# Optimization experiments

Hardware: AMD Instinct MI355X
Metric: run time of the kernel (lower is better)

Reference implementation:

```python
import jax, jax.numpy as jnp
import numpy as np

T, B, I, H, NC = 1024, 256, 128, 64, 10


def _lstm_cell(x_t, h, c, W_ih, W_hh, b):
    # PyTorch gate order: i, f, g, o. gates: [B, 4H]
    gates = x_t @ W_ih.T + h @ W_hh.T + b
    i, f, g, o = jnp.split(gates, 4, axis=-1)
    i = jax.nn.sigmoid(i)
    f = jax.nn.sigmoid(f)
    g = jnp.tanh(g)
    o = jax.nn.sigmoid(o)
    c = f * c + i * g
    h = o * jnp.tanh(c)
    return h, c


def setup_inputs() -> dict:
    key = jax.random.key(0)
    ks = jax.random.split(key, 12)
    s = 1.0 / np.sqrt(H)  # PyTorch LSTM init scale
    d = {
        "x": jax.random.normal(ks[0], (T, B, I), dtype=jnp.float32),
        # forward direction LSTM params
        "W_ih_f": jax.random.uniform(ks[1], (4 * H, I), minval=-s, maxval=s, dtype=jnp.float32),
        "W_hh_f": jax.random.uniform(ks[2], (4 * H, H), minval=-s, maxval=s, dtype=jnp.float32),
        "b_f": jax.random.uniform(ks[3], (4 * H,), minval=-s, maxval=s, dtype=jnp.float32),
        # reverse direction LSTM params
        "W_ih_r": jax.random.uniform(ks[4], (4 * H, I), minval=-s, maxval=s, dtype=jnp.float32),
        "W_hh_r": jax.random.uniform(ks[5], (4 * H, H), minval=-s, maxval=s, dtype=jnp.float32),
        "b_r": jax.random.uniform(ks[6], (4 * H,), minval=-s, maxval=s, dtype=jnp.float32),
        # MLP head: 2H -> 64 -> 32 -> NC
        "fc1_w": jax.random.normal(ks[7], (64, 2 * H), dtype=jnp.float32) * 0.05,
        "fc1_b": jnp.zeros((64,), dtype=jnp.float32),
        "fc2_w": jax.random.normal(ks[8], (32, 64), dtype=jnp.float32) * 0.05,
        "fc2_b": jnp.zeros((32,), dtype=jnp.float32),
        "fc3_w": jax.random.normal(ks[9], (NC, 32), dtype=jnp.float32) * 0.05,
        "fc3_b": jnp.zeros((NC,), dtype=jnp.float32),
    }
    return d


def _forward(x, W_ih_f, W_hh_f, b_f, W_ih_r, W_hh_r, b_r,
             fc1_w, fc1_b, fc2_w, fc2_b, fc3_w, fc3_b):
    Bsz = x.shape[1]
    h0 = jnp.zeros((Bsz, H), dtype=x.dtype)
    c0 = jnp.zeros((Bsz, H), dtype=x.dtype)

    # Forward direction: only the final hidden state is needed (output[-1] fwd half).
    def fwd_step(carry, x_t):
        h, c = carry
        h, c = _lstm_cell(x_t, h, c, W_ih_f, W_hh_f, b_f)
        return (h, c), None

    (h_fwd_last, _), _ = jax.lax.scan(fwd_step, (h0, c0), x)

    # Reverse direction: output[-1] reverse half is the hidden after processing
    # x[-1] first (reverse scan starts from the last timestep with zero state).
    h_bwd_last, _ = _lstm_cell(x[-1], h0, c0, W_ih_r, W_hh_r, b_r)

    h_cat = jnp.concatenate([h_fwd_last, h_bwd_last], axis=-1)  # [B, 2H]

    h1 = jax.nn.relu(h_cat @ fc1_w.T + fc1_b)
    h2 = jax.nn.relu(h1 @ fc2_w.T + fc2_b)
    out = h2 @ fc3_w.T + fc3_b  # [B, NC]
    return out


def reference(x, W_ih_f, W_hh_f, b_f, W_ih_r, W_hh_r, b_r,
              fc1_w, fc1_b, fc2_w, fc2_b, fc3_w, fc3_b):
    return _forward(x, W_ih_f, W_hh_f, b_f, W_ih_r, W_hh_r, b_r,
                    fc1_w, fc1_b, fc2_w, fc2_b, fc3_w, fc3_b)
```

## Files before the change

### kernel.cpp

```cpp
#include <hip/hip_runtime.h>
#include <math.h>

#define T_LEN 1024
#define B_SZ  256
#define I_SZ  128
#define H_SZ  64
#define G_SZ  256
#define SUB   32

typedef float f32x8 __attribute__((ext_vector_type(8)));

__device__ __forceinline__ float fast_tanh(float x) {
    float e = __expf(-2.0f * fabsf(x));
    float r = (1.0f - e) * __builtin_amdgcn_rcpf(1.0f + e);
    return copysignf(r, x);
}

#define LD8PIN(V, P)                                                        \
    {   float4 t0_ = *reinterpret_cast<const float4*>(P);                   \
        float4 t1_ = *reinterpret_cast<const float4*>((P) + 4);             \
        V = (f32x8){t0_.x, t0_.y, t0_.z, t0_.w, t1_.x, t1_.y, t1_.z, t1_.w};\
        asm volatile("" : "+v"(V)); }

#define HD(V, M)                                                            \
    {   const float4 ha_ = hp[2*(M)], hb_ = hp[2*(M) + 1];                  \
        a0 = fmaf(ha_.x, V[0], a0); a1 = fmaf(ha_.y, V[1], a1);             \
        a2 = fmaf(ha_.z, V[2], a2); a3 = fmaf(ha_.w, V[3], a3);             \
        a0 = fmaf(hb_.x, V[4], a0); a1 = fmaf(hb_.y, V[5], a1);             \
        a2 = fmaf(hb_.z, V[6], a2); a3 = fmaf(hb_.w, V[7], a3); }

__device__ __forceinline__ int swz(int c) { return c + 4 * (c >> 5); }

__global__ __launch_bounds__(256, 2) void xg_gemm(
    const float* __restrict__ xch,
    const float* __restrict__ W_ih,
    const float* __restrict__ bias,
    float* __restrict__ XG)
{
    const int tid = threadIdx.x;
    const int tx  = tid & 15;
    const int ty  = tid >> 4;
    const int mt  = blockIdx.x;
    const int nt  = blockIdx.y;

    __shared__ __align__(16) float as[32][140];
    __shared__ __align__(16) float bs[32][140];

    const int n0 = nt * 128 + tx * 8;
    float4 bia = *reinterpret_cast<const float4*>(&bias[n0]);
    float4 bib = *reinterpret_cast<const float4*>(&bias[n0 + 4]);

    float acc[8][8];
#pragma unroll
    for (int r = 0; r < 8; ++r)
#pragma unroll
        for (int cc = 0; cc < 8; ++cc) acc[r][cc] = 0.0f;

    const int srow = tid >> 3;
    const int skk  = (tid & 7) * 4;

    for (int ks = 0; ks < 4; ++ks) {
        const int k0 = ks * 32;
        __syncthreads();
#pragma unroll
        for (int i = 0; i < 4; ++i) {
            const int mr = srow + 32 * i;
            float4 xa = *reinterpret_cast<const float4*>(
                &xch[(size_t)(mt * 128 + mr) * I_SZ + k0 + skk]);
            as[skk + 0][swz(mr)] = xa.x; as[skk + 1][swz(mr)] = xa.y;
            as[skk + 2][swz(mr)] = xa.z; as[skk + 3][swz(mr)] = xa.w;
            float4 wa = *reinterpret_cast<const float4*>(
                &W_ih[(size_t)(nt * 128 + mr) * I_SZ + k0 + skk]);
            bs[skk + 0][swz(mr)] = wa.x; bs[skk + 1][swz(mr)] = wa.y;
            bs[skk + 2][swz(mr)] = wa.z; bs[skk + 3][swz(mr)] = wa.w;
        }
        __syncthreads();

#pragma unroll 8
        for (int kk = 0; kk < 32; ++kk) {
            const float4 a0 = *reinterpret_cast<const float4*>(&as[kk][swz(ty * 8)]);
            const float4 a1 = *reinterpret_cast<const float4*>(&as[kk][swz(ty * 8) + 4]);
            const float4 b0 = *reinterpret_cast<const float4*>(&bs[kk][swz(tx * 8)]);
            const float4 b1 = *reinterpret_cast<const float4*>(&bs[kk][swz(tx * 8) + 4]);
            const float av[8] = {a0.x, a0.y, a0.z, a0.w, a1.x, a1.y, a1.z, a1.w};
            const float bv[8] = {b0.x, b0.y, b0.z, b0.w, b1.x, b1.y, b1.z, b1.w};
#pragma unroll
            for (int r = 0; r < 8; ++r)
#pragma unroll
                for (int cc = 0; cc < 8; ++cc)
                    acc[r][cc] = fmaf(av[r], bv[cc], acc[r][cc]);
        }
    }

#pragma unroll
    for (int r = 0; r < 8; ++r) {
        const size_t m = (size_t)(mt * 128 + ty * 8 + r);
        float4 o0 = {acc[r][0] + bia.x, acc[r][1] + bia.y,
                     acc[r][2] + bia.z, acc[r][3] + bia.w};
        float4 o1 = {acc[r][4] + bib.x, acc[r][5] + bib.y,
                     acc[r][6] + bib.z, acc[r][7] + bib.w};
        *reinterpret_cast<float4*>(&XG[m * G_SZ + n0])     = o0;
        *reinterpret_cast<float4*>(&XG[m * G_SZ + n0 + 4]) = o1;
    }
}

__global__ __launch_bounds__(512, 1) void lstm_rec(
    const float* __restrict__ XG,
    const float* __restrict__ W_hh,
    float* __restrict__ h_state,
    float* __restrict__ c_state,
    int TC, int first)
{
    const int b    = blockIdx.x;
    const int t    = threadIdx.x;
    const int row  = t >> 1;
    const int half = t & 1;
    const int g    = row >> 6;
    const int w    = t >> 6;
    const int l    = t & 63;

    __shared__ __align__(16) float xgl[2][SUB][G_SZ];
    __shared__ __align__(16) float hsb[8][H_SZ];
    __shared__ float gs[2][G_SZ];

    const float* ur = W_hh + row * H_SZ + half * 32;
    f32x8 w0, w1, w2, w3;
    LD8PIN(w0, ur) LD8PIN(w1, ur + 8) LD8PIN(w2, ur + 16) LD8PIN(w3, ur + 24)

    float c = first ? 0.0f : c_state[b * H_SZ + l];
    hsb[w][l] = first ? 0.0f : h_state[b * H_SZ + l];

    {
        float* xf = &xgl[0][0][0];
#pragma unroll
        for (int i = 0; i < 4; ++i) {
            const int F = t + 512 * i;
            const int r = F >> 6, cw = F & 63;
            *reinterpret_cast<float4*>(xf + 4 * F) =
                *reinterpret_cast<const float4*>(
                    XG + ((size_t)r * B_SZ + b) * G_SZ + 4 * cw);
        }
    }
    __syncthreads();

    const bool isg = (g == 2);
    const int nsub = TC / SUB;
    int db = 0;
    float h = 0.0f;

    for (int sub = 0; sub < nsub; ++sub) {
        const int cur = sub & 1;
        if (sub + 1 < nsub) {
            float* xf = &xgl[cur ^ 1][0][0];
#pragma unroll
            for (int i = 0; i < 4; ++i) {
                const int F = t + 512 * i;
                const int r = (F >> 6) + (sub + 1) * SUB, cw = F & 63;
                *reinterpret_cast<float4*>(xf + 4 * F) =
                    *reinterpret_cast<const float4*>(
                        XG + ((size_t)r * B_SZ + b) * G_SZ + 4 * cw);
            }
        }

#pragma unroll 4
        for (int ts = 0; ts < SUB; ++ts) {
            const float xg = xgl[cur][ts][row];
            const float4* hp =
                reinterpret_cast<const float4*>(&hsb[w][half * 32]);
            float a0 = 0.0f, a1 = 0.0f, a2 = 0.0f, a3 = 0.0f;
            HD(w0, 0) HD(w1, 1) HD(w2, 2) HD(w3, 3)
            float acc = (a0 + a1) + (a2 + a3);
            acc += __shfl_xor(acc, 1, 64);
            acc += xg;

            const float arg = isg ? (-2.0f * acc) : (-acc);
            const float e = __expf(arg);
            const float r = __builtin_amdgcn_rcpf(1.0f + e);
            const float a = isg ? (1.0f - e) * r : r;

            if (half == 0) gs[db][row] = a;
            __syncthreads();

            const float ig = gs[db][l];
            const float fg = gs[db][H_SZ + l];
            const float gg = gs[db][2 * H_SZ + l];
            const float og = gs[db][3 * H_SZ + l];
            c = fmaf(fg, c, ig * gg);
            h = og * fast_tanh(c);
            hsb[w][l] = h;
            db ^= 1;
        }
    }

    if (t < H_SZ) {
        h_state[b * H_SZ + t] = h;
        c_state[b * H_SZ + t] = c;
    }
}

__global__ __launch_bounds__(256, 1) void lstm_tail(
    const float* __restrict__ x_last,
    const float* __restrict__ W_ih_r,
    const float* __restrict__ b_r,
    const float* __restrict__ h_fwd,
    const float* __restrict__ fc1_w,
    const float* __restrict__ fc1_b,
    const float* __restrict__ fc2_w,
    const float* __restrict__ fc2_b,
    const float* __restrict__ fc3_w,
    const float* __restrict__ fc3_b,
    float* __restrict__ out)
{
    const int b = blockIdx.x;
    const int j = threadIdx.x;

    __shared__ float xs[I_SZ];
    __shared__ float gs[G_SZ];
    __shared__ float hc[2 * H_SZ];
    __shared__ float h1[64];
    __shared__ float h2[32];

    if (j < I_SZ) xs[j] = x_last[(size_t)b * I_SZ + j];
    if (j < H_SZ) hc[j] = h_fwd[b * H_SZ + j];
    __syncthreads();

    float a0 = b_r[j], a1 = 0.0f, a2 = 0.0f, a3 = 0.0f;
    const float* wrow = W_ih_r + j * I_SZ;
#pragma unroll
    for (int kk = 0; kk < I_SZ; kk += 4) {
        float4 wv = *reinterpret_cast<const float4*>(wrow + kk);
        a0 = fmaf(xs[kk + 0], wv.x, a0);
        a1 = fmaf(xs[kk + 1], wv.y, a1);
        a2 = fmaf(xs[kk + 2], wv.z, a2);
        a3 = fmaf(xs[kk + 3], wv.w, a3);
    }
    const float acc = (a0 + a1) + (a2 + a3);
    const int gate = j >> 6;
    gs[j] = (gate == 2) ? tanhf(acc) : 1.0f / (1.0f + expf(-acc));
    __syncthreads();

    if (j < H_SZ) {
        const float cc = gs[j] * gs[2 * H_SZ + j];
        hc[H_SZ + j] = gs[3 * H_SZ + j] * tanhf(cc);
    }
    __syncthreads();

    if (j < 64) {
        float s0 = fc1_b[j], s1 = 0.0f, s2 = 0.0f, s3 = 0.0f;
        const float* w = fc1_w + j * 128;
#pragma unroll
    for (int kk = 0; kk < 128; kk += 4) {
            float4 wv = *reinterpret_cast<const float4*>(w + kk);
            s0 = fmaf(hc[kk + 0], wv.x, s0);
            s1 = fmaf(hc[kk + 1], wv.y, s1);
            s2 = fmaf(hc[kk + 2], wv.z, s2);
            s3 = fmaf(hc[kk + 3], wv.w, s3);
        }
        h1[j] = fmaxf((s0 + s1) + (s2 + s3), 0.0f);
    }
    __syncthreads();

    if (j < 32) {
        float s0 = fc2_b[j], s1 = 0.0f, s2 = 0.0f, s3 = 0.0f;
        const float* w = fc2_w + j * 64;
#pragma unroll
        for (int kk = 0; kk < 64; kk += 4) {
            float4 wv = *reinterpret_cast<const float4*>(w + kk);
            s0 = fmaf(h1[kk + 0], wv.x, s0);
            s1 = fmaf(h1[kk + 1], wv.y, s1);
            s2 = fmaf(h1[kk + 2], wv.z, s2);
            s3 = fmaf(h1[kk + 3], wv.w, s3);
        }
        h2[j] = fmaxf((s0 + s1) + (s2 + s3), 0.0f);
    }
    __syncthreads();

    if (j < 10) {
        float s = fc3_b[j];
#pragma unroll
        for (int kk = 0; kk < 32; ++kk) s = fmaf(h2[kk], fc3_w[j * 32 + kk], s);
        out[b * 10 + j] = s;
    }
}

extern "C" void kernel_launch(void* const* d_in, const int* in_sizes, int n_in,
                              void* d_out, int out_size, void* d_ws, size_t ws_size,
                              hipStream_t stream) {
    const float* x      = (const float*)d_in[0];
    const float* W_ih_f = (const float*)d_in[1];
    const float* W_hh_f = (const float*)d_in[2];
    const float* b_f    = (const float*)d_in[3];
    const float* W_ih_r = (const float*)d_in[4];
    const float* b_r    = (const float*)d_in[6];
    const float* fc1_w  = (const float*)d_in[7];
    const float* fc1_b  = (const float*)d_in[8];
    const float* fc2_w  = (const float*)d_in[9];
    const float* fc2_b  = (const float*)d_in[10];
    const float* fc3_w  = (const float*)d_in[11];
    const float* fc3_b  = (const float*)d_in[12];
    float* out = (float*)d_out;

    int TC = 1024;
    while (TC > 64 &&
           (size_t)TC * B_SZ * G_SZ * 4 + 2 * B_SZ * H_SZ * 4 > ws_size)
        TC >>= 1;

    float* XG      = (float*)d_ws;
    float* h_state = (float*)((char*)d_ws + (size_t)TC * B_SZ * G_SZ * 4);
    float* c_state = h_state + B_SZ * H_SZ;

    const int NCH = T_LEN / TC;
    for (int ch = 0; ch < NCH; ++ch) {
        const float* xch = x + (size_t)ch * TC * B_SZ * I_SZ;
        hipLaunchKernelGGL(xg_gemm, dim3(TC * B_SZ / 128, 2), dim3(256), 0,
                           stream, xch, W_ih_f, b_f, XG);
        hipLaunchKernelGGL(lstm_rec, dim3(B_SZ), dim3(512), 0, stream,
                           XG, W_hh_f, h_state, c_state, TC, ch == 0 ? 1 : 0);
    }

    const float* x_last = x + (size_t)(T_LEN - 1) * B_SZ * I_SZ;
    hipLaunchKernelGGL(lstm_tail, dim3(B_SZ), dim3(256), 0, stream,
                       x_last, W_ih_r, b_r, h_state,
                       fc1_w, fc1_b, fc2_w, fc2_b, fc3_w, fc3_b, out);
}
```

Baseline: 685.8 us.

## Broadcast hidden state via readlane and use one thread per gate row

The recurrent kernel drops from 512 to 256 threads per block, so each thread now holds a full 64-wide W_hh row in registers instead of half a row. The cross-lane shuffle that combined the two halves is removed. The hidden state is no longer written to and read back from a per-wave LDS buffer; each wave broadcasts h from its own lanes with readlane into scalar registers. This removes LDS traffic and a shuffle from the serial per-timestep critical path, at the cost of 64 serialized readlanes and longer per-thread FMA chains, plus doubled weight register pressure.

```diff
diff --git a/kernel.cpp b/kernel.cpp
--- a/kernel.cpp
+++ b/kernel.cpp
@@ -22,12 +22,23 @@
         V = (f32x8){t0_.x, t0_.y, t0_.z, t0_.w, t1_.x, t1_.y, t1_.z, t1_.w};\
         asm volatile("" : "+v"(V)); }
 
-#define HD(V, M)                                                            \
-    {   const float4 ha_ = hp[2*(M)], hb_ = hp[2*(M) + 1];                  \
-        a0 = fmaf(ha_.x, V[0], a0); a1 = fmaf(ha_.y, V[1], a1);             \
-        a2 = fmaf(ha_.z, V[2], a2); a3 = fmaf(ha_.w, V[3], a3);             \
-        a0 = fmaf(hb_.x, V[4], a0); a1 = fmaf(hb_.y, V[5], a1);             \
-        a2 = fmaf(hb_.z, V[6], a2); a3 = fmaf(hb_.w, V[7], a3); }
+#define RL8(V, K)                                                           \
+    {   unsigned r0_ = __builtin_amdgcn_readlane(hu, (K) + 0);              \
+        unsigned r1_ = __builtin_amdgcn_readlane(hu, (K) + 1);              \
+        unsigned r2_ = __builtin_amdgcn_readlane(hu, (K) + 2);              \
+        unsigned r3_ = __builtin_amdgcn_readlane(hu, (K) + 3);              \
+        a0 = fmaf(__uint_as_float(r0_), V[0], a0);                          \
+        a1 = fmaf(__uint_as_float(r1_), V[1], a1);                          \
+        a2 = fmaf(__uint_as_float(r2_), V[2], a2);                          \
+        a3 = fmaf(__uint_as_float(r3_), V[3], a3);                          \
+        unsigned r4_ = __builtin_amdgcn_readlane(hu, (K) + 4);              \
+        unsigned r5_ = __builtin_amdgcn_readlane(hu, (K) + 5);              \
+        unsigned r6_ = __builtin_amdgcn_readlane(hu, (K) + 6);              \
+        unsigned r7_ = __builtin_amdgcn_readlane(hu, (K) + 7);              \
+        a0 = fmaf(__uint_as_float(r4_), V[4], a0);                          \
+        a1 = fmaf(__uint_as_float(r5_), V[5], a1);                          \
+        a2 = fmaf(__uint_as_float(r6_), V[6], a2);                          \
+        a3 = fmaf(__uint_as_float(r7_), V[7], a3); }
 
 __device__ __forceinline__ int swz(int c) { return c + 4 * (c >> 5); }
 
@@ -104,37 +115,35 @@
     }
 }
 
-__global__ __launch_bounds__(512, 1) void lstm_rec(
+__global__ __launch_bounds__(256, 1) void lstm_rec(
     const float* __restrict__ XG,
     const float* __restrict__ W_hh,
     float* __restrict__ h_state,
     float* __restrict__ c_state,
     int TC, int first)
 {
-    const int b    = blockIdx.x;
-    const int t    = threadIdx.x;
-    const int row  = t >> 1;
-    const int half = t & 1;
-    const int g    = row >> 6;
-    const int w    = t >> 6;
-    const int l    = t & 63;
+    const int b = blockIdx.x;
+    const int t = threadIdx.x;
+    const int l = t & 63;
+    const int g = t >> 6;
+    const int row = t;
 
     __shared__ __align__(16) float xgl[2][SUB][G_SZ];
-    __shared__ __align__(16) float hsb[8][H_SZ];
     __shared__ float gs[2][G_SZ];
 
-    const float* ur = W_hh + row * H_SZ + half * 32;
-    f32x8 w0, w1, w2, w3;
-    LD8PIN(w0, ur) LD8PIN(w1, ur + 8) LD8PIN(w2, ur + 16) LD8PIN(w3, ur + 24)
-
+    const float* ur = W_hh + row * H_SZ;
+    f32x8 w0, w1, w2, w3, w4, w5, w6, w7;
+    LD8PIN(w0, ur)      LD8PIN(w1, ur +  8) LD8PIN(w2, ur + 16) LD8PIN(w3, ur + 24)
+    LD8PIN(w4, ur + 32) LD8PIN(w5, ur + 40) LD8PIN(w6, ur + 48) LD8PIN(w7, ur + 56)
+
+    float h = first ? 0.0f : h_state[b * H_SZ + l];
     float c = first ? 0.0f : c_state[b * H_SZ + l];
-    hsb[w][l] = first ? 0.0f : h_state[b * H_SZ + l];
 
     {
         float* xf = &xgl[0][0][0];
 #pragma unroll
-        for (int i = 0; i < 4; ++i) {
-            const int F = t + 512 * i;
+        for (int i = 0; i < 8; ++i) {
+            const int F = t + 256 * i;
             const int r = F >> 6, cw = F & 63;
             *reinterpret_cast<float4*>(xf + 4 * F) =
                 *reinterpret_cast<const float4*>(
@@ -146,15 +155,14 @@
     const bool isg = (g == 2);
     const int nsub = TC / SUB;
     int db = 0;
-    float h = 0.0f;
 
     for (int sub = 0; sub < nsub; ++sub) {
         const int cur = sub & 1;
         if (sub + 1 < nsub) {
             float* xf = &xgl[cur ^ 1][0][0];
 #pragma unroll
-            for (int i = 0; i < 4; ++i) {
-                const int F = t + 512 * i;
+            for (int i = 0; i < 8; ++i) {
+                const int F = t + 256 * i;
                 const int r = (F >> 6) + (sub + 1) * SUB, cw = F & 63;
                 *reinterpret_cast<float4*>(xf + 4 * F) =
                     *reinterpret_cast<const float4*>(
@@ -164,21 +172,19 @@
 
 #pragma unroll 4
         for (int ts = 0; ts < SUB; ++ts) {
-            const float xg = xgl[cur][ts][row];
-            const float4* hp =
-                reinterpret_cast<const float4*>(&hsb[w][half * 32]);
-            float a0 = 0.0f, a1 = 0.0f, a2 = 0.0f, a3 = 0.0f;
-            HD(w0, 0) HD(w1, 1) HD(w2, 2) HD(w3, 3)
-            float acc = (a0 + a1) + (a2 + a3);
-            acc += __shfl_xor(acc, 1, 64);
-            acc += xg;
+            const unsigned hu = __float_as_uint(h);
+            float a0 = xgl[cur][ts][row];
+            float a1 = 0.0f, a2 = 0.0f, a3 = 0.0f;
+            RL8(w0,  0) RL8(w1,  8) RL8(w2, 16) RL8(w3, 24)
+            RL8(w4, 32) RL8(w5, 40) RL8(w6, 48) RL8(w7, 56)
+            const float acc = (a0 + a1) + (a2 + a3);
 
             const float arg = isg ? (-2.0f * acc) : (-acc);
             const float e = __expf(arg);
             const float r = __builtin_amdgcn_rcpf(1.0f + e);
             const float a = isg ? (1.0f - e) * r : r;
 
-            if (half == 0) gs[db][row] = a;
+            gs[db][row] = a;
             __syncthreads();
 
             const float ig = gs[db][l];
@@ -187,7 +193,6 @@
             const float og = gs[db][3 * H_SZ + l];
             c = fmaf(fg, c, ig * gg);
             h = og * fast_tanh(c);
-            hsb[w][l] = h;
             db ^= 1;
         }
     }
@@ -249,7 +254,7 @@
         float s0 = fc1_b[j], s1 = 0.0f, s2 = 0.0f, s3 = 0.0f;
         const float* w = fc1_w + j * 128;
 #pragma unroll
-    for (int kk = 0; kk < 128; kk += 4) {
+        for (int kk = 0; kk < 128; kk += 4) {
             float4 wv = *reinterpret_cast<const float4*>(w + kk);
             s0 = fmaf(hc[kk + 0], wv.x, s0);
             s1 = fmaf(hc[kk + 1], wv.y, s1);
@@ -314,7 +319,7 @@
         const float* xch = x + (size_t)ch * TC * B_SZ * I_SZ;
         hipLaunchKernelGGL(xg_gemm, dim3(TC * B_SZ / 128, 2), dim3(256), 0,
                            stream, xch, W_ih_f, b_f, XG);
-        hipLaunchKernelGGL(lstm_rec, dim3(B_SZ), dim3(512), 0, stream,
+        hipLaunchKernelGGL(lstm_rec, dim3(B_SZ), dim3(256), 0, stream,
                            XG, W_hh_f, h_state, c_state, TC, ch == 0 ? 1 : 0);
     }
 
```

Measured after the change: 645.0 us. 6.0% less time.
